# Kernel optimization log

Measured on AMD Instinct MI355X. Metric: run time of the kernel, lower is better.

## Reference

```python
import jax, jax.numpy as jnp
import numpy as np

WINDOW, HOP = 20, 10   # SplitSignal_cplx(2, window_size=20, hop_length=10)
EPS = 1e-6             # eigenvalue clip for matrix log
RIDGE = 1e-3           # SPD ridge to keep matrices positive definite


def sparsemax(z):
    # Closed-form sparsemax projection onto the simplex (Martins & Astudillo 2016),
    # mirroring use_sparsemax_as_convex_layer (QP projection onto the simplex).
    zs = jnp.sort(z)[::-1]
    k = jnp.arange(1, z.shape[0] + 1, dtype=z.dtype)
    zc = jnp.cumsum(zs)
    support = 1.0 + k * zs > zc
    kz_i = jnp.sum(support).astype(jnp.int32)
    kz = kz_i.astype(z.dtype)
    tau = (zc[kz_i - 1] - 1.0) / kz
    return jnp.maximum(z - tau, 0.0)


def _sym(S):
    return 0.5 * (S + jnp.swapaxes(S, -1, -2))


def logm(S):
    # batched symmetric matrix log via eigh (LogEig / barycenter log-map)
    w, V = jnp.linalg.eigh(_sym(S))
    lw = jnp.log(jnp.maximum(w, EPS))
    return jnp.einsum('...ij,...j,...kj->...ik', V, lw, V)


def expm(S):
    w, V = jnp.linalg.eigh(_sym(S))
    return jnp.einsum('...ij,...j,...kj->...ik', V, jnp.exp(w), V)


def frame_signal(x):
    # x: [B, 2, T] -> frames [B, 2*n_win, WINDOW]  (SplitSignal)
    B, Cc, T = x.shape
    n_win = (T - WINDOW) // HOP + 1
    idx = jnp.arange(n_win)[:, None] * HOP + jnp.arange(WINDOW)[None, :]
    f = x[:, :, idx]                      # [B, 2, n_win, WINDOW]
    return f.reshape(B, Cc * n_win, WINDOW)


def covpool(f):
    # covariance pooling over frames -> SPD [B, WINDOW, WINDOW]
    N = f.shape[1]
    f = f - f.mean(axis=1, keepdims=True)
    cov = jnp.einsum('bnd,bne->bde', f, f) / (N - 1)
    return cov + RIDGE * jnp.eye(WINDOW, dtype=f.dtype)


def cell(S, W, alpha):
    # One DARTS-style SPD cell: candidate BiMap ops + per-channel weighted
    # Riemannian (log-Euclidean) barycenter  G = expm(sum_k w_k logm(op_k(S))).
    # S: [B, C, d, d];  W: [2, K, d, do] (2 branches -> channel doubling);
    # alpha: [K] architecture logits.
    w = sparsemax(alpha)                               # [K]
    cand = jnp.einsum('mkji,bcjl,mkln->mkbcin', W, S, W)  # [2, K, B, C, do, do]
    do = cand.shape[-1]
    cand = cand + RIDGE * jnp.eye(do, dtype=S.dtype)
    L = logm(cand)                                     # log-map of every candidate
    G = expm(jnp.einsum('k,mkbcij->mbcij', w, L))      # weighted barycenter [2,B,C,do,do]
    B = S.shape[0]
    return jnp.moveaxis(G, 0, 1).reshape(B, -1, do, do)  # channels double: [B, 2C, do, do]


def reference(x, W_stem, W_op0, W_op1, W_op2, alphas, W_cls, b_cls):
    f = frame_signal(x)                                # [B, 798, 20]
    cov = covpool(f)                                   # [B, 20, 20]
    # stem BiMap: W^T S W
    S = jnp.einsum('ji,bjk,kl->bil', W_stem, cov, W_stem)[:, None]  # [B,1,20,20]
    S = S + RIDGE * jnp.eye(WINDOW, dtype=x.dtype)
    S = cell(S, W_op0, alphas[0])                      # [B, 2, 10, 10] (reduce 20->10)
    S = cell(S, W_op1, alphas[1])                      # [B, 4, 10, 10]
    S = cell(S, W_op2, alphas[2])                      # [B, 8, 10, 10]
    out = logm(S).reshape(S.shape[0], -1)              # LogEig + flatten -> [B, 800]
    return out @ W_cls + b_cls


def setup_inputs() -> dict:
    key = jax.random.key(0)
    ks = jax.random.split(key, 8)
    B, T = 2048, 4000
    d_in, d_out, K, n_cls = 20, 10, 6, 10
    x = jax.random.normal(ks[0], (B, 2, T), jnp.float32)
    W_stem = jax.random.normal(ks[1], (d_in, d_in), jnp.float32) / np.sqrt(d_in)
    W_op0 = jax.random.normal(ks[2], (2, K, d_in, d_out), jnp.float32) / np.sqrt(d_in)
    W_op1 = jax.random.normal(ks[3], (2, K, d_out, d_out), jnp.float32) / np.sqrt(d_out)
    W_op2 = jax.random.normal(ks[4], (2, K, d_out, d_out), jnp.float32) / np.sqrt(d_out)
    alphas = 0.001 * jax.random.normal(ks[5], (3, K), jnp.float32)
    W_cls = jax.random.normal(ks[6], (8 * d_out * d_out, n_cls), jnp.float32) * 0.02
    b_cls = jnp.zeros((n_cls,), jnp.float32)
    return dict(x=x, W_stem=W_stem, W_op0=W_op0, W_op1=W_op1, W_op2=W_op2,
                alphas=alphas, W_cls=W_cls, b_cls=b_cls)
```

## Files before the change

### kernel.cpp

```cpp
#include <hip/hip_runtime.h>
#include <math.h>

#define WIN   20
#define NWIN  399
#define NCH   2
#define TLEN  4000
#define NFR   798
#define KOPS  6
#define NB    2048
#define EPSV  1e-6f
#define RIDGE 1e-3f

#define TIX(i,j) ((i)*10 - (i)*((i)+1)/2 + (j))

__device__ __forceinline__ float frcp(float x){float r;asm("v_rcp_f32 %0, %1":"=v"(r):"v"(x));return r;}
__device__ __forceinline__ float frsq(float x){float r;asm("v_rsq_f32 %0, %1":"=v"(r):"v"(x));return r;}
__device__ __forceinline__ float fsqr(float x){float r;asm("v_sqrt_f32 %0, %1":"=v"(r):"v"(x));return r;}

__device__ __forceinline__ void jacobi10(float* A, float* V) {
#pragma unroll
  for (int i = 0; i < 100; i++) V[i] = 0.f;
#pragma unroll
  for (int i = 0; i < 10; i++) V[i * 11] = 1.f;

  for (int sweep = 0; sweep < 7; ++sweep) {
    float off = 0.f, dia = 0.f;
#pragma unroll
    for (int p = 0; p < 10; p++) {
      float d = A[TIX(p, p)];
      dia = fmaf(d, d, dia);
#pragma unroll
      for (int q = p + 1; q < 10; q++) { float o = A[TIX(p, q)]; off = fmaf(o, o, off); }
    }
    float fro2 = dia + 2.f * off;
    if (__ballot(off > 1e-11f * fro2) == 0ull) break;
    float skipthr = 1e-12f * fro2;

#pragma unroll
    for (int p = 0; p < 10; p++) {
#pragma unroll
      for (int q = p + 1; q < 10; q++) {
        float apq = A[TIX(p, q)];
        if (__ballot(apq * apq > skipthr) == 0ull) continue;
        float app = A[TIX(p, p)];
        float aqq = A[TIX(q, q)];
        bool rot = fabsf(apq) > 1e-30f;
        float theta = (aqq - app) * frcp(rot ? 2.f * apq : 1.f);
        float t = copysignf(frcp(fabsf(theta) + fsqr(fmaf(theta, theta, 1.f))), theta);
        t = rot ? t : 0.f;
        float c = frsq(fmaf(t, t, 1.f));
        float s = t * c;
#pragma unroll
        for (int j = 0; j < 10; j++) {
          if (j == p || j == q) continue;
          const int jp = (j < p) ? TIX(j, p) : TIX(p, j);
          const int jq = (j < q) ? TIX(j, q) : TIX(q, j);
          float ajp = A[jp], ajq = A[jq];
          A[jp] = fmaf(c, ajp, -s * ajq);
          A[jq] = fmaf(s, ajp, c * ajq);
        }
        A[TIX(p, p)] = fmaf(-t, apq, A[TIX(p, p)]);
        A[TIX(q, q)] = fmaf(t, apq, A[TIX(q, q)]);
        A[TIX(p, q)] = 0.0f;
#pragma unroll
        for (int i = 0; i < 10; i++) {
          float vip = V[i * 10 + p], viq = V[i * 10 + q];
          V[i * 10 + p] = fmaf(c, vip, -s * viq);
          V[i * 10 + q] = fmaf(s, vip, c * viq);
        }
      }
    }
  }
}

__global__ __launch_bounds__(256) void k_cov_stem(const float* __restrict__ x,
                                                  const float* __restrict__ Wst,
                                                  float* __restrict__ Sout) {
  __shared__ float xl[NCH * TLEN];
  __shared__ float pT[2][NCH][100];
  __shared__ float pQ[2][NCH][100];
  __shared__ float bsum[NCH][10];
  __shared__ float b0v[NCH][10];
  __shared__ float b399v[NCH][10];
  __shared__ float cov[400];
  __shared__ float wst[400];
  __shared__ float tmp[400];
  int b = blockIdx.x, tid = threadIdx.x;
  const float4* xg = (const float4*)(x + (size_t)b * NCH * TLEN);
  float4* xl4 = (float4*)xl;
  for (int i = tid; i < NCH * TLEN / 4; i += 256) xl4[i] = xg[i];
  for (int i = tid; i < 400; i += 256) wst[i] = Wst[i];
  __syncthreads();

  if (tid < 200) {
    int grp = tid / 100;
    int c = (tid % 100) / 50;
    int r = tid % 50;
    int seg = r / 25, tile = r % 25;
    int d0 = (tile / 5) * 2, e0 = (tile % 5) * 2;
    const float* xc = xl + c * TLEN;
    int i0 = seg * 200;
    int i1 = grp ? ((seg == 1) ? 399 : 200) : (i0 + 200);
    int eoff = grp ? 10 : 0;
    float a00 = 0.f, a01 = 0.f, a10 = 0.f, a11 = 0.f;
    for (int i = i0; i < i1; i++) {
      float2 bd = *(const float2*)(xc + i * 10 + d0);
      float2 be = *(const float2*)(xc + i * 10 + eoff + e0);
      a00 = fmaf(bd.x, be.x, a00); a01 = fmaf(bd.x, be.y, a01);
      a10 = fmaf(bd.y, be.x, a10); a11 = fmaf(bd.y, be.y, a11);
    }
    float* dst = grp ? &pQ[seg][c][0] : &pT[seg][c][0];
    dst[d0 * 10 + e0] = a00;
    dst[d0 * 10 + e0 + 1] = a01;
    dst[(d0 + 1) * 10 + e0] = a10;
    dst[(d0 + 1) * 10 + e0 + 1] = a11;
  } else if (tid >= 200 && tid < 220) {
    int c = (tid - 200) / 10, d = (tid - 200) % 10;
    const float* xc = xl + c * TLEN;
    float s = 0.f;
    for (int i = 0; i < 400; i++) s += xc[i * 10 + d];
    bsum[c][d] = s;
    b0v[c][d] = xc[d];
    b399v[c][d] = xc[3990 + d];
  }
  __syncthreads();

  const float invN = 1.0f / (float)NFR;
  const float invN1 = 1.0f / (float)(NFR - 1);
  for (int o = tid; o < 400; o += 256) {
    int d = o / 20, e = o % 20;
    int dl = d % 10, el = e % 10;
    float s2;
    if (d < 10 && e < 10)
      s2 = (pT[0][0][dl * 10 + el] + pT[1][0][dl * 10 + el] - b399v[0][dl] * b399v[0][el]) +
           (pT[0][1][dl * 10 + el] + pT[1][1][dl * 10 + el] - b399v[1][dl] * b399v[1][el]);
    else if (d >= 10 && e >= 10)
      s2 = (pT[0][0][dl * 10 + el] + pT[1][0][dl * 10 + el] - b0v[0][dl] * b0v[0][el]) +
           (pT[0][1][dl * 10 + el] + pT[1][1][dl * 10 + el] - b0v[1][dl] * b0v[1][el]);
    else if (d < 10)
      s2 = pQ[0][0][dl * 10 + el] + pQ[1][0][dl * 10 + el] +
           pQ[0][1][dl * 10 + el] + pQ[1][1][dl * 10 + el];
    else
      s2 = pQ[0][0][el * 10 + dl] + pQ[1][0][el * 10 + dl] +
           pQ[0][1][el * 10 + dl] + pQ[1][1][el * 10 + dl];
    float md = (d < 10) ? (bsum[0][dl] - b399v[0][dl] + bsum[1][dl] - b399v[1][dl])
                        : (bsum[0][dl] - b0v[0][dl] + bsum[1][dl] - b0v[1][dl]);
    float me = (e < 10) ? (bsum[0][el] - b399v[0][el] + bsum[1][el] - b399v[1][el])
                        : (bsum[0][el] - b0v[0][el] + bsum[1][el] - b0v[1][el]);
    float v = (s2 - (float)NFR * (md * invN) * (me * invN)) * invN1;
    if (d == e) v += RIDGE;
    cov[o] = v;
  }
  __syncthreads();
  for (int o = tid; o < 400; o += 256) {
    int j = o / 20, l = o % 20;
    float acc = 0.f;
    for (int k2 = 0; k2 < 20; k2++) acc = fmaf(cov[j * 20 + k2], wst[k2 * 20 + l], acc);
    tmp[o] = acc;
  }
  __syncthreads();
  for (int o = tid; o < 400; o += 256) {
    int i = o / 20, l = o % 20;
    float acc = 0.f;
    for (int j = 0; j < 20; j++) acc = fmaf(wst[j * 20 + i], tmp[j * 20 + l], acc);
    if (i == l) acc += RIDGE;
    Sout[b * 400 + o] = acc;
  }
}

__global__ __launch_bounds__(256) void k_cand20(const float* __restrict__ Sin,
                                                const float* __restrict__ Wop,
                                                float* __restrict__ cand, int BC) {
  const int DIN = 20;
  __shared__ float Sl[DIN * DIN];
  __shared__ float Wl[12 * DIN * 10];
  __shared__ float Tl[12 * DIN * 10];
  int bc = blockIdx.x, tid = threadIdx.x;
  for (int i = tid; i < DIN * DIN; i += 256) Sl[i] = Sin[bc * DIN * DIN + i];
  for (int i = tid; i < 12 * DIN * 10; i += 256) Wl[i] = Wop[i];
  __syncthreads();
  for (int o = tid; o < 12 * DIN * 10; o += 256) {
    int mk = o / (DIN * 10);
    int r = o % (DIN * 10);
    int j = r / 10, n = r % 10;
    float acc = 0.f;
    for (int l = 0; l < DIN; l++) acc = fmaf(Sl[j * DIN + l], Wl[mk * DIN * 10 + l * 10 + n], acc);
    Tl[o] = acc;
  }
  __syncthreads();
  int NM = 12 * BC;
  for (int o = tid; o < 12 * 55; o += 256) {
    int mk = o / 55, t = o % 55;
    int t0 = t, i = 0;
    while (t0 >= 10 - i) { t0 -= 10 - i; i++; }
    int n = i + t0;
    float acc = 0.f;
    for (int j = 0; j < DIN; j++)
      acc = fmaf(Wl[mk * DIN * 10 + j * 10 + i], Tl[mk * DIN * 10 + j * 10 + n], acc);
    if (i == n) acc += RIDGE;
    cand[t * NM + mk * BC + bc] = acc;
  }
}

__device__ __forceinline__ void logm_epilogue(float* A, float* V,
                                              float* __restrict__ cand, int NM, int mat) {
  float f[10];
#pragma unroll
  for (int r = 0; r < 10; r++) f[r] = __logf(fmaxf(A[TIX(r, r)], EPSV));
#pragma unroll
  for (int i = 0; i < 10; i++) {
    float w[10];
#pragma unroll
    for (int r = 0; r < 10; r++) w[r] = V[i * 10 + r] * f[r];
#pragma unroll
    for (int n = i; n < 10; n++) {
      float acc = 0.f;
#pragma unroll
      for (int r = 0; r < 10; r++) acc = fmaf(w[r], V[n * 10 + r], acc);
      cand[TIX(i, n) * NM + mat] = acc;
    }
  }
}

__global__ __launch_bounds__(256) void k_logm(float* __restrict__ cand, int NM) {
  int mat = blockIdx.x * 256 + threadIdx.x;
  float A[55];
#pragma unroll
  for (int t = 0; t < 55; t++) A[t] = cand[t * NM + mat];
  float V[100];
  jacobi10(A, V);
  logm_epilogue(A, V, cand, NM, mat);
}

template <int BC>
__global__ __launch_bounds__(256) void k_candlogm(const float* __restrict__ Sin,
                                                  const float* __restrict__ Wop,
                                                  float* __restrict__ cand) {
  __shared__ float Wl[1200];
  int tid = threadIdx.x;
  for (int i = tid; i < 1200; i += 256) Wl[i] = Wop[i];
  __syncthreads();
  const int NM = 12 * BC;
  int mat = blockIdx.x * 256 + tid;
  int mk = mat / BC, bc = mat % BC;
  const float* Wm = Wl + mk * 100;
  const float* Sb = Sin + bc;

  float U[100];
#pragma unroll
  for (int i = 0; i < 100; i++) U[i] = 0.f;
#pragma unroll
  for (int j = 0; j < 10; j++) {
    float sr[10];
#pragma unroll
    for (int l = 0; l < 10; l++) sr[l] = Sb[(j * 10 + l) * BC];
    float wr[10];
#pragma unroll
    for (int i = 0; i < 10; i++) wr[i] = Wm[j * 10 + i];
#pragma unroll
    for (int i = 0; i < 10; i++)
#pragma unroll
      for (int l = 0; l < 10; l++) U[i * 10 + l] = fmaf(wr[i], sr[l], U[i * 10 + l]);
  }
  float A[55];
#pragma unroll
  for (int t = 0; t < 55; t++) A[t] = 0.f;
#pragma unroll
  for (int i = 0; i < 10; i++) A[TIX(i, i)] = RIDGE;
#pragma unroll
  for (int l = 0; l < 10; l++) {
    float wr[10];
#pragma unroll
    for (int n = 0; n < 10; n++) wr[n] = Wm[l * 10 + n];
#pragma unroll
    for (int i = 0; i < 10; i++) {
      float u = U[i * 10 + l];
#pragma unroll
      for (int n = i; n < 10; n++) A[TIX(i, n)] = fmaf(u, wr[n], A[TIX(i, n)]);
    }
  }
  float V[100];
  jacobi10(A, V);
  logm_epilogue(A, V, cand, NM, mat);
}

__device__ __forceinline__ void sparsemax6(const float* __restrict__ a, int row, float* w) {
  float z[KOPS], zs[KOPS];
#pragma unroll
  for (int i = 0; i < KOPS; i++) { z[i] = a[row * KOPS + i]; zs[i] = z[i]; }
#pragma unroll
  for (int i = 0; i < KOPS; i++)
#pragma unroll
    for (int j = i + 1; j < KOPS; j++)
      if (zs[j] > zs[i]) { float tm = zs[i]; zs[i] = zs[j]; zs[j] = tm; }
  float acc = 0.f, zcp = 1.f; float cnt = 1.f;
#pragma unroll
  for (int i = 0; i < KOPS; i++) {
    acc += zs[i];
    if (1.0f + (float)(i + 1) * zs[i] > acc) { cnt = (float)(i + 1); zcp = acc; }
  }
  float tau = (zcp - 1.0f) / cnt;
#pragma unroll
  for (int i = 0; i < KOPS; i++) w[i] = fmaxf(z[i] - tau, 0.0f);
}

template <int BC, int C>
__global__ __launch_bounds__(64) void k_expm(const float* __restrict__ L,
                                             const float* __restrict__ alphas, int row,
                                             float* __restrict__ Sout) {
  const int NM = 12 * BC;
  const int NE = 2 * BC;
  int id = blockIdx.x * 64 + threadIdx.x;
  int m = id / BC;
  int bc = id % BC;
  float w[KOPS];
  sparsemax6(alphas, row, w);
  float A[55];
#pragma unroll
  for (int t = 0; t < 55; t++) {
    float acc = 0.f;
#pragma unroll
    for (int k2 = 0; k2 < KOPS; k2++) acc = fmaf(w[k2], L[t * NM + (m * KOPS + k2) * BC + bc], acc);
    A[t] = acc;
  }
  float V[100];
  jacobi10(A, V);
  float f[10];
#pragma unroll
  for (int r = 0; r < 10; r++) f[r] = __expf(A[TIX(r, r)]);
  int b = bc / C, c = bc % C;
  int idm = b * 2 * C + m * C + c;
  float* out = Sout + idm;
#pragma unroll
  for (int i = 0; i < 10; i++) {
    float wv[10];
#pragma unroll
    for (int r = 0; r < 10; r++) wv[r] = V[i * 10 + r] * f[r];
#pragma unroll
    for (int n = i; n < 10; n++) {
      float acc = 0.f;
#pragma unroll
      for (int r = 0; r < 10; r++) acc = fmaf(wv[r], V[n * 10 + r], acc);
      out[(i * 10 + n) * NE] = acc;
      if (n != i) out[(n * 10 + i) * NE] = acc;
    }
  }
}

__global__ __launch_bounds__(64) void k_final(const float* __restrict__ Sin,
                                              const float* __restrict__ Wc,
                                              const float* __restrict__ bcv,
                                              float* __restrict__ out) {
  const int NE = 8 * NB;
  int id = blockIdx.x * 64 + threadIdx.x;
  int ch = id & 7;
  float A[55];
#pragma unroll
  for (int i = 0; i < 10; i++)
#pragma unroll
    for (int n = i; n < 10; n++) A[TIX(i, n)] = Sin[(i * 10 + n) * NE + id];
  float V[100];
  jacobi10(A, V);
  float f[10];
#pragma unroll
  for (int r = 0; r < 10; r++) f[r] = __logf(fmaxf(A[TIX(r, r)], EPSV));
  float acc[10];
#pragma unroll
  for (int c2 = 0; c2 < 10; c2++) acc[c2] = 0.f;
  const float* wbase = Wc + ch * 1000;
#pragma unroll
  for (int i = 0; i < 10; i++) {
    float wv[10];
#pragma unroll
    for (int r = 0; r < 10; r++) wv[r] = V[i * 10 + r] * f[r];
#pragma unroll
    for (int n = 0; n < 10; n++) {
      float lv = 0.f;
#pragma unroll
      for (int r = 0; r < 10; r++) lv = fmaf(wv[r], V[n * 10 + r], lv);
      const float* wrow = wbase + (i * 10 + n) * 10;
#pragma unroll
      for (int h = 0; h < 5; h++) {
        float2 wc2 = *(const float2*)(wrow + 2 * h);
        acc[2 * h]     = fmaf(lv, wc2.x, acc[2 * h]);
        acc[2 * h + 1] = fmaf(lv, wc2.y, acc[2 * h + 1]);
      }
    }
  }
#pragma unroll
  for (int mk = 1; mk < 8; mk <<= 1) {
#pragma unroll
    for (int c2 = 0; c2 < 10; c2++) acc[c2] += __shfl_xor(acc[c2], mk, 8);
  }
  if (ch == 0) {
    int b = id >> 3;
#pragma unroll
    for (int c2 = 0; c2 < 10; c2++) out[b * 10 + c2] = acc[c2] + bcv[c2];
  }
}

extern "C" void kernel_launch(void* const* d_in, const int* in_sizes, int n_in,
                              void* d_out, int out_size, void* d_ws, size_t ws_size,
                              hipStream_t stream) {
  const float* x      = (const float*)d_in[0];
  const float* Wst    = (const float*)d_in[1];
  const float* Wop0   = (const float*)d_in[2];
  const float* Wop1   = (const float*)d_in[3];
  const float* Wop2   = (const float*)d_in[4];
  const float* alphas = (const float*)d_in[5];
  const float* Wcls   = (const float*)d_in[6];
  const float* bcls   = (const float*)d_in[7];
  float* out = (float*)d_out;

  float* ws   = (float*)d_ws;
  float* Sa   = ws;
  float* Sb   = Sa + (size_t)NB * 800;
  float* cand = Sb + (size_t)NB * 800;

  k_cov_stem<<<NB, 256, 0, stream>>>(x, Wst, Sa);

  k_cand20<<<NB, 256, 0, stream>>>(Sa, Wop0, cand, NB);
  k_logm<<<(12 * NB) / 256, 256, 0, stream>>>(cand, 12 * NB);
  k_expm<NB, 1><<<(2 * NB) / 64, 64, 0, stream>>>(cand, alphas, 0, Sb);

  k_candlogm<NB * 2><<<(12 * NB * 2) / 256, 256, 0, stream>>>(Sb, Wop1, cand);
  k_expm<NB * 2, 2><<<(4 * NB) / 64, 64, 0, stream>>>(cand, alphas, 1, Sa);

  k_candlogm<NB * 4><<<(12 * NB * 4) / 256, 256, 0, stream>>>(Sa, Wop2, cand);
  k_expm<NB * 4, 4><<<(8 * NB) / 64, 64, 0, stream>>>(cand, alphas, 2, Sb);

  k_final<<<(8 * NB) / 64, 64, 0, stream>>>(Sb, Wcls, bcls, out);
}
```

Before: 470.2 us.

## Skip last-cell expm and final logm by using weighted log-sum directly

The final stage previously ran expm on the last cell's weighted log-barycenter, then logm on the result before the classifier. Since logm(expm(Z)) equals Z for symmetric Z, the new kernel forms the sparsemax-weighted sum of candidate logs and feeds it straight into the classifier. This removes one expm kernel launch and two batched 10x10 Jacobi eigendecompositions, along with an intermediate buffer round trip. Results can differ slightly where the EPS clip would have altered tiny eigenvalues of the expm output.

```diff
diff --git a/kernel.cpp b/kernel.cpp
--- a/kernel.cpp
+++ b/kernel.cpp
@@ -347,37 +347,38 @@
   }
 }
 
-__global__ __launch_bounds__(64) void k_final(const float* __restrict__ Sin,
-                                              const float* __restrict__ Wc,
-                                              const float* __restrict__ bcv,
-                                              float* __restrict__ out) {
-  const int NE = 8 * NB;
+__global__ __launch_bounds__(64) void k_final_direct(const float* __restrict__ L,
+                                                     const float* __restrict__ alphas,
+                                                     const float* __restrict__ Wc,
+                                                     const float* __restrict__ bcv,
+                                                     float* __restrict__ out) {
+  const int BC = 4 * NB;
+  const int NM = 12 * BC;
   int id = blockIdx.x * 64 + threadIdx.x;
   int ch = id & 7;
-  float A[55];
-#pragma unroll
-  for (int i = 0; i < 10; i++)
-#pragma unroll
-    for (int n = i; n < 10; n++) A[TIX(i, n)] = Sin[(i * 10 + n) * NE + id];
-  float V[100];
-  jacobi10(A, V);
-  float f[10];
-#pragma unroll
-  for (int r = 0; r < 10; r++) f[r] = __logf(fmaxf(A[TIX(r, r)], EPSV));
+  int b = id >> 3;
+  int m = ch >> 2, j = ch & 3;
+  int bc = b * 4 + j;
+  float w[KOPS];
+  sparsemax6(alphas, 2, w);
+  const float* Lb = L + (size_t)(m * KOPS) * BC + bc;
+  float Z[55];
+#pragma unroll
+  for (int t = 0; t < 55; t++) {
+    float acc = 0.f;
+#pragma unroll
+    for (int k2 = 0; k2 < KOPS; k2++) acc = fmaf(w[k2], Lb[(size_t)t * NM + k2 * BC], acc);
+    Z[t] = acc;
+  }
   float acc[10];
 #pragma unroll
   for (int c2 = 0; c2 < 10; c2++) acc[c2] = 0.f;
   const float* wbase = Wc + ch * 1000;
 #pragma unroll
   for (int i = 0; i < 10; i++) {
-    float wv[10];
-#pragma unroll
-    for (int r = 0; r < 10; r++) wv[r] = V[i * 10 + r] * f[r];
 #pragma unroll
     for (int n = 0; n < 10; n++) {
-      float lv = 0.f;
-#pragma unroll
-      for (int r = 0; r < 10; r++) lv = fmaf(wv[r], V[n * 10 + r], lv);
+      float lv = (i <= n) ? Z[TIX(i, n)] : Z[TIX(n, i)];
       const float* wrow = wbase + (i * 10 + n) * 10;
 #pragma unroll
       for (int h = 0; h < 5; h++) {
@@ -393,7 +394,6 @@
     for (int c2 = 0; c2 < 10; c2++) acc[c2] += __shfl_xor(acc[c2], mk, 8);
   }
   if (ch == 0) {
-    int b = id >> 3;
 #pragma unroll
     for (int c2 = 0; c2 < 10; c2++) out[b * 10 + c2] = acc[c2] + bcv[c2];
   }
@@ -427,7 +427,6 @@
   k_expm<NB * 2, 2><<<(4 * NB) / 64, 64, 0, stream>>>(cand, alphas, 1, Sa);
 
   k_candlogm<NB * 4><<<(12 * NB * 4) / 256, 256, 0, stream>>>(Sa, Wop2, cand);
-  k_expm<NB * 4, 4><<<(8 * NB) / 64, 64, 0, stream>>>(cand, alphas, 2, Sb);
-
-  k_final<<<(8 * NB) / 64, 64, 0, stream>>>(Sb, Wcls, bcls, out);
-}
+
+  k_final_direct<<<(8 * NB) / 64, 64, 0, stream>>>(cand, alphas, Wcls, bcls, out);
+}
```

Result: faster. 408.7 us (-13.1%).
